# Performance work log

Hardware: AMD Instinct MI355X
Metric: run time of the kernel (lower is better)

## Reference

```python
import jax, jax.numpy as jnp
import numpy as np

N_QUBITS = 16
N_LAYERS = 4
N_ACTIONS = 6
BATCH = 512


def _apply_1q(state, U, wire):
    """Apply a single-qubit gate U to `wire` of batched state [B,2,...,2].
    U is [2,2] (shared) or [B,2,2] (per-sample)."""
    s = jnp.moveaxis(state, wire + 1, -1)
    if U.ndim == 2:
        s = jnp.einsum('ij,b...j->b...i', U, s)
    else:
        s = jnp.einsum('bij,b...j->b...i', U, s)
    return jnp.moveaxis(s, -1, wire + 1)


def _ry(theta):
    # RY(theta); theta scalar or [B]
    c = jnp.cos(theta / 2).astype(jnp.complex64)
    s = jnp.sin(theta / 2).astype(jnp.complex64)
    return jnp.stack([jnp.stack([c, -s], -1), jnp.stack([s, c], -1)], -2)


def _rot(phi, theta, omega):
    # PennyLane Rot = RZ(omega) RY(theta) RZ(phi)
    c = jnp.cos(theta / 2)
    s = jnp.sin(theta / 2)
    ep = jnp.exp(-0.5j * (phi + omega).astype(jnp.complex64))
    em = jnp.exp(-0.5j * (phi - omega).astype(jnp.complex64))
    m00 = ep * c
    m01 = -jnp.conj(em) * s
    m10 = em * s
    m11 = jnp.conj(ep) * c
    return jnp.stack([jnp.stack([m00, m01], -1), jnp.stack([m10, m11], -1)], -2)


def _cz_factor(wire):
    # diagonal CZ phase on wires (wire, wire+1): diag(1,1,1,-1)
    f = jnp.array([1, 1, 1, -1], dtype=jnp.complex64).reshape(2, 2)
    shape = (1,) + (1,) * wire + (2, 2) + (1,) * (N_QUBITS - wire - 2)
    return f.reshape(shape)


def _circuit(x, weights):
    # x: [B, n_qubits] angles; weights: [L, n_qubits, 3]
    B = x.shape[0]
    state = jnp.zeros((B,) + (2,) * N_QUBITS, dtype=jnp.complex64)
    state = state.at[(slice(None),) + (0,) * N_QUBITS].set(1.0)
    # AngleEmbedding: RY(x_i) on wire i (per-sample angles)
    for i in range(N_QUBITS):
        state = _apply_1q(state, _ry(x[:, i]), i)
    for l in range(N_LAYERS):
        for i in range(N_QUBITS):
            state = _apply_1q(state, _rot(weights[l, i, 0], weights[l, i, 1], weights[l, i, 2]), i)
        for i in range(N_QUBITS - 1):
            state = state * _cz_factor(i)
    probs = state.real ** 2 + state.imag ** 2  # [B,2,...,2]
    zs = []
    all_axes = tuple(range(1, N_QUBITS + 1))
    for i in range(N_QUBITS):
        pi = jnp.sum(probs, axis=tuple(a for a in all_axes if a != i + 1))  # [B,2]
        zs.append(pi[:, 0] - pi[:, 1])
    return jnp.stack(zs, axis=-1)  # [B, n_qubits] expval <Z_i>


def setup_inputs() -> dict:
    key = jax.random.key(0)
    k1, k2, k3, k4 = jax.random.split(key, 4)
    x = jax.random.uniform(k1, (BATCH, N_QUBITS), dtype=jnp.float32) * np.float32(np.pi)
    weights = jax.random.normal(k2, (N_LAYERS, N_QUBITS, 3), dtype=jnp.float32)
    fc_w = jax.random.normal(k3, (N_ACTIONS, N_QUBITS), dtype=jnp.float32) / np.float32(np.sqrt(N_QUBITS))
    fc_b = jax.random.normal(k4, (N_ACTIONS,), dtype=jnp.float32) * 0.01
    return {"x": x, "weights": weights, "fc_w": fc_w, "fc_b": fc_b}


def reference(x, weights, fc_w, fc_b):
    z = _circuit(x, weights).astype(jnp.float32)  # [B, n_qubits]
    return z @ fc_w.T + fc_b  # [B, n_actions]
```

## Files before the change

### kernel.cpp

```cpp
#include <hip/hip_runtime.h>

#define N_QUBITS 16
#define N_LAYERS 4
#define N_ACTIONS 6
#define BATCH 512


__global__ __launch_bounds__(1024, 4)
void qdqn_fused_kernel(const float* __restrict__ x,
                       const float* __restrict__ wt,
                       const float* __restrict__ fw,
                       const float* __restrict__ fb,
                       float* __restrict__ out)
{
    __shared__ float4 mats[4][N_QUBITS][2];
    __shared__ float zsh[N_QUBITS];

    const int tid = threadIdx.x;
    const int b   = blockIdx.x;

    if (tid < 64) {
        const int w = tid & 15;
        const int g = tid >> 4;
        float4 M0, M1;
        if (g == 0) {
            const float phi = wt[(0 * N_QUBITS + w) * 3 + 0];
            const float th  = wt[(0 * N_QUBITS + w) * 3 + 1];
            float sp, cp, st, ct;
            sincosf(0.5f * phi, &sp, &cp);
            sincosf(0.5f * th,  &st, &ct);
            const float w00r =  ct * cp, w00i = -ct * sp;
            const float w01r = -st * cp, w01i = -st * sp;
            const float w10r =  st * cp, w10i = -st * sp;
            const float w11r =  ct * cp, w11i =  ct * sp;
            float sx, cx;
            sincosf(0.5f * x[b * N_QUBITS + w], &sx, &cx);
            M0.x =  w00r * cx + w01r * sx;  M0.y =  w00i * cx + w01i * sx;
            M0.z = -w00r * sx + w01r * cx;  M0.w = -w00i * sx + w01i * cx;
            M1.x =  w10r * cx + w11r * sx;  M1.y =  w10i * cx + w11i * sx;
            M1.z = -w10r * sx + w11r * cx;  M1.w = -w10i * sx + w11i * cx;
        } else {
            const float al = wt[((g - 1) * N_QUBITS + w) * 3 + 2]
                           + wt[(g * N_QUBITS + w) * 3 + 0];
            const float th = wt[(g * N_QUBITS + w) * 3 + 1];
            float sa, ca, st, ct;
            sincosf(0.5f * al, &sa, &ca);
            sincosf(0.5f * th, &st, &ct);
            M0 = make_float4( ct * ca, -ct * sa, -st * ca, -st * sa);
            M1 = make_float4( st * ca, -st * sa,  ct * ca,  ct * sa);
        }
        mats[g][w][0] = M0;
        mats[g][w][1] = M1;
    }
    __syncthreads();

    const int lane = tid & 63;
    const int qi   = tid >> 6;
    int s = qi - 3;
    s = s < 0 ? 0 : (s > N_QUBITS - 7 ? N_QUBITS - 7 : s);
    const int jm = qi - s;

    float ar0 = (lane == 0) ? 1.0f : 0.0f, ai0 = 0.0f;
    float ar1 = 0.0f, ai1 = 0.0f;

    const int n0 = lane << 1, n1 = n0 | 1;
    const float czs0 = (__popc((n0 & (n0 >> 1)) & 0x3F) & 1) ? -1.0f : 1.0f;
    const float czs1 = (__popc((n1 & (n1 >> 1)) & 0x3F) & 1) ? -1.0f : 1.0f;

    auto applyM = [&](int j, float4 m0, float4 m1) {
        if (j == 0) {
            const float nr0 = m0.x*ar0 - m0.y*ai0 + m0.z*ar1 - m0.w*ai1;
            const float ni0 = m0.x*ai0 + m0.y*ar0 + m0.z*ai1 + m0.w*ar1;
            const float nr1 = m1.x*ar0 - m1.y*ai0 + m1.z*ar1 - m1.w*ai1;
            const float ni1 = m1.x*ai0 + m1.y*ar0 + m1.z*ai1 + m1.w*ar1;
            ar0 = nr0; ai0 = ni0; ar1 = nr1; ai1 = ni1;
        } else {
            const int  m  = 1 << (j - 1);
            const bool hi = (lane & m) != 0;
            const float dr = hi ? m1.z : m0.x;
            const float di = hi ? m1.w : m0.y;
            const float og = hi ? m1.x : m0.z;
            const float oi = hi ? m1.y : m0.w;
            {
                const float pr = __shfl_xor(ar0, m, 64);
                const float pi = __shfl_xor(ai0, m, 64);
                const float nr = dr*ar0 - di*ai0 + og*pr - oi*pi;
                const float ni = dr*ai0 + di*ar0 + og*pi + oi*pr;
                ar0 = nr; ai0 = ni;
            }
            {
                const float pr = __shfl_xor(ar1, m, 64);
                const float pi = __shfl_xor(ai1, m, 64);
                const float nr = dr*ar1 - di*ai1 + og*pr - oi*pi;
                const float ni = dr*ai1 + di*ar1 + og*pi + oi*pr;
                ar1 = nr; ai1 = ni;
            }
        }
    };

#pragma unroll
    for (int l = 0; l < 4; ++l) {
        const int rad = 3 - l;
#pragma unroll
        for (int dj = -3; dj <= 3; ++dj) {
            if (dj < -rad || dj > rad) continue;
            const int j = jm + dj;
            if (j >= 0 && j <= 6) {
                const int w = s + j;
                applyM(j, mats[l][w][0], mats[l][w][1]);
            }
        }
        if (l < 3) { ar0 *= czs0; ai0 *= czs0; ar1 *= czs1; ai1 *= czs1; }
    }

    const float sm0 = ((n0 >> jm) & 1) ? -1.0f : 1.0f;
    const float sm1 = ((n1 >> jm) & 1) ? -1.0f : 1.0f;
    float p = sm0 * (ar0*ar0 + ai0*ai0) + sm1 * (ar1*ar1 + ai1*ai1);
#pragma unroll
    for (int off = 32; off > 0; off >>= 1)
        p += __shfl_xor(p, off, 64);
    if (lane == 0) zsh[qi] = p;
    __syncthreads();

    if (tid < N_ACTIONS) {
        float acc = fb[tid];
#pragma unroll
        for (int i = 0; i < N_QUBITS; ++i)
            acc += zsh[i] * fw[tid * N_QUBITS + i];
        out[b * N_ACTIONS + tid] = acc;
    }
}

extern "C" void kernel_launch(void* const* d_in, const int* in_sizes, int n_in,
                              void* d_out, int out_size, void* d_ws, size_t ws_size,
                              hipStream_t stream) {
    const float* x    = (const float*)d_in[0];
    const float* wts  = (const float*)d_in[1];
    const float* fc_w = (const float*)d_in[2];
    const float* fc_b = (const float*)d_in[3];
    float* out = (float*)d_out;

    qdqn_fused_kernel<<<BATCH, 1024, 0, stream>>>(x, wts, fc_w, fc_b, out);
}
```

Baseline: 68.14 us.

## Split into prep kernel and 4-block-per-sample main kernel with atomic output

Gate matrix computation moves into a separate prep kernel that writes the per-sample first-layer matrices and the shared later-layer matrices to workspace, and also initialises the output with the bias. The main kernel now launches 2048 blocks of 256 threads, four blocks per sample, each handling four qubits' light-cone simulation. It loads matrices from workspace, applies the gates through fully unrolled macros with row-indexed matrix loads, and accumulates partial FC results with atomicAdd. This aims to improve occupancy and scheduling granularity, and to remove the redundant per-block trig work. In exchange it adds a second launch, workspace traffic, and atomics whose summation order is nondeterministic.

```diff
diff --git a/kernel.cpp b/kernel.cpp
--- a/kernel.cpp
+++ b/kernel.cpp
@@ -1,64 +1,78 @@
 #include <hip/hip_runtime.h>
 
-#define N_QUBITS 16
-#define N_LAYERS 4
-#define N_ACTIONS 6
+#define NQ 16
+#define NL 4
+#define NA 6
 #define BATCH 512
 
+#define A1_OFF 1024
 
-__global__ __launch_bounds__(1024, 4)
-void qdqn_fused_kernel(const float* __restrict__ x,
-                       const float* __restrict__ wt,
-                       const float* __restrict__ fw,
-                       const float* __restrict__ fb,
-                       float* __restrict__ out)
+__global__ __launch_bounds__(256)
+void prep_kernel(const float* __restrict__ x,
+                 const float* __restrict__ wt,
+                 const float* __restrict__ fb,
+                 float4* __restrict__ ws,
+                 float* __restrict__ out)
 {
-    __shared__ float4 mats[4][N_QUBITS][2];
-    __shared__ float zsh[N_QUBITS];
-
-    const int tid = threadIdx.x;
-    const int b   = blockIdx.x;
-
-    if (tid < 64) {
-        const int w = tid & 15;
-        const int g = tid >> 4;
-        float4 M0, M1;
-        if (g == 0) {
-            const float phi = wt[(0 * N_QUBITS + w) * 3 + 0];
-            const float th  = wt[(0 * N_QUBITS + w) * 3 + 1];
-            float sp, cp, st, ct;
-            sincosf(0.5f * phi, &sp, &cp);
-            sincosf(0.5f * th,  &st, &ct);
-            const float w00r =  ct * cp, w00i = -ct * sp;
-            const float w01r = -st * cp, w01i = -st * sp;
-            const float w10r =  st * cp, w10i = -st * sp;
-            const float w11r =  ct * cp, w11i =  ct * sp;
-            float sx, cx;
-            sincosf(0.5f * x[b * N_QUBITS + w], &sx, &cx);
-            M0.x =  w00r * cx + w01r * sx;  M0.y =  w00i * cx + w01i * sx;
-            M0.z = -w00r * sx + w01r * cx;  M0.w = -w00i * sx + w01i * cx;
-            M1.x =  w10r * cx + w11r * sx;  M1.y =  w10i * cx + w11i * sx;
-            M1.z = -w10r * sx + w11r * cx;  M1.w = -w10i * sx + w11i * cx;
-        } else {
-            const float al = wt[((g - 1) * N_QUBITS + w) * 3 + 2]
-                           + wt[(g * N_QUBITS + w) * 3 + 0];
-            const float th = wt[(g * N_QUBITS + w) * 3 + 1];
+    const int tid = threadIdx.x, blk = blockIdx.x;
+    if (blk < 32) {
+        const int t = blk * 256 + tid;
+        const int b = t >> 4, w = t & 15;
+        const float phi = wt[w * 3 + 0], th = wt[w * 3 + 1];
+        float sp, cp, st, ct, sx, cx;
+        sincosf(0.5f * phi, &sp, &cp);
+        sincosf(0.5f * th,  &st, &ct);
+        sincosf(0.5f * x[b * NQ + w], &sx, &cx);
+        const float w00r =  ct * cp, w00i = -ct * sp;
+        const float w01r = -st * cp, w01i = -st * sp;
+        const float w10r =  st * cp, w10i = -st * sp;
+        const float w11r =  ct * cp, w11i =  ct * sp;
+        const float a00r =  w00r * cx + w01r * sx, a00i =  w00i * cx + w01i * sx;
+        const float a01r = -w00r * sx + w01r * cx, a01i = -w00i * sx + w01i * cx;
+        const float a10r =  w10r * cx + w11r * sx, a10i =  w10i * cx + w11i * sx;
+        const float a11r = -w10r * sx + w11r * cx, a11i = -w10i * sx + w11i * cx;
+        ws[A1_OFF + t * 2 + 0] = make_float4(a00r, a00i, a01r, a01i);
+        ws[A1_OFF + t * 2 + 1] = make_float4(a11r, a11i, a10r, a10i);
+    } else if (blk == 32) {
+        if (tid < 48) {
+            const int g = tid >> 4, w = tid & 15;
+            const int l = g + 1;
+            const float al = wt[((l - 1) * NQ + w) * 3 + 2] + wt[(l * NQ + w) * 3 + 0];
+            const float th = wt[(l * NQ + w) * 3 + 1];
             float sa, ca, st, ct;
             sincosf(0.5f * al, &sa, &ca);
             sincosf(0.5f * th, &st, &ct);
-            M0 = make_float4( ct * ca, -ct * sa, -st * ca, -st * sa);
-            M1 = make_float4( st * ca, -st * sa,  ct * ca,  ct * sa);
+            ws[tid * 2 + 0] = make_float4(ct * ca, -ct * sa, -st * ca, -st * sa);
+            ws[tid * 2 + 1] = make_float4(ct * ca,  ct * sa,  st * ca, -st * sa);
         }
-        mats[g][w][0] = M0;
-        mats[g][w][1] = M1;
+    } else {
+        const int t = (blk - 33) * 256 + tid;
+        if (t < BATCH * NA) out[t] = fb[t - (t / NA) * NA];
+    }
+}
+
+
+__global__ __launch_bounds__(256, 8)
+void qmain_kernel(const float4* __restrict__ ws,
+                  const float* __restrict__ fw,
+                  float* __restrict__ out)
+{
+    __shared__ float4 lm[4][NQ][2];
+    __shared__ float zsh[4];
+
+    const int tid = threadIdx.x;
+    const int b   = blockIdx.x >> 2;
+
+    if (tid < 128) {
+        const int g = tid >> 5;
+        ((float4*)lm)[tid] = (g == 0) ? ws[A1_OFF + (b << 5) + tid]
+                                      : ws[tid - 32];
     }
     __syncthreads();
 
     const int lane = tid & 63;
-    const int qi   = tid >> 6;
-    int s = qi - 3;
-    s = s < 0 ? 0 : (s > N_QUBITS - 7 ? N_QUBITS - 7 : s);
-    const int jm = qi - s;
+    const int wv   = tid >> 6;
+    const int qi   = ((blockIdx.x & 3) << 2) | wv;
 
     float ar0 = (lane == 0) ? 1.0f : 0.0f, ai0 = 0.0f;
     float ar1 = 0.0f, ai1 = 0.0f;
@@ -67,67 +81,60 @@
     const float czs0 = (__popc((n0 & (n0 >> 1)) & 0x3F) & 1) ? -1.0f : 1.0f;
     const float czs1 = (__popc((n1 & (n1 >> 1)) & 0x3F) & 1) ? -1.0f : 1.0f;
 
-    auto applyM = [&](int j, float4 m0, float4 m1) {
-        if (j == 0) {
-            const float nr0 = m0.x*ar0 - m0.y*ai0 + m0.z*ar1 - m0.w*ai1;
-            const float ni0 = m0.x*ai0 + m0.y*ar0 + m0.z*ai1 + m0.w*ar1;
-            const float nr1 = m1.x*ar0 - m1.y*ai0 + m1.z*ar1 - m1.w*ai1;
-            const float ni1 = m1.x*ai0 + m1.y*ar0 + m1.z*ai1 + m1.w*ar1;
-            ar0 = nr0; ai0 = ni0; ar1 = nr1; ai1 = ni1;
-        } else {
-            const int  m  = 1 << (j - 1);
-            const bool hi = (lane & m) != 0;
-            const float dr = hi ? m1.z : m0.x;
-            const float di = hi ? m1.w : m0.y;
-            const float og = hi ? m1.x : m0.z;
-            const float oi = hi ? m1.y : m0.w;
-            {
-                const float pr = __shfl_xor(ar0, m, 64);
-                const float pi = __shfl_xor(ai0, m, 64);
-                const float nr = dr*ar0 - di*ai0 + og*pr - oi*pi;
-                const float ni = dr*ai0 + di*ar0 + og*pi + oi*pr;
-                ar0 = nr; ai0 = ni;
-            }
-            {
-                const float pr = __shfl_xor(ar1, m, 64);
-                const float pi = __shfl_xor(ai1, m, 64);
-                const float nr = dr*ar1 - di*ai1 + og*pr - oi*pi;
-                const float ni = dr*ai1 + di*ar1 + og*pi + oi*pr;
-                ar1 = nr; ai1 = ni;
-            }
-        }
-    };
+#define GATE(J, G) do {                                                        \
+    const int w_ = qi + (J) - 3;                                               \
+    if (0 <= w_ && w_ < NQ) {                                                  \
+        if ((J) == 0) {                                                        \
+            const float4 r0 = lm[G][w_][0], r1 = lm[G][w_][1];                 \
+            const float nr0 = r0.x*ar0 - r0.y*ai0 + r0.z*ar1 - r0.w*ai1;       \
+            const float ni0 = r0.x*ai0 + r0.y*ar0 + r0.z*ai1 + r0.w*ar1;       \
+            const float nr1 = r1.z*ar0 - r1.w*ai0 + r1.x*ar1 - r1.y*ai1;       \
+            const float ni1 = r1.z*ai0 + r1.w*ar0 + r1.x*ai1 + r1.y*ar1;       \
+            ar0 = nr0; ai0 = ni0; ar1 = nr1; ai1 = ni1;                        \
+        } else {                                                               \
+            const int m_   = 1 << ((J) - 1);                                   \
+            const int row_ = (lane >> ((J) - 1)) & 1;                          \
+            const float4 c = lm[G][w_][row_];                                  \
+            const float pr0 = __shfl_xor(ar0, m_, 64);                         \
+            const float pi0 = __shfl_xor(ai0, m_, 64);                         \
+            const float pr1 = __shfl_xor(ar1, m_, 64);                         \
+            const float pi1 = __shfl_xor(ai1, m_, 64);                         \
+            const float t0r = c.x*ar0 - c.y*ai0 + c.z*pr0 - c.w*pi0;           \
+            const float t0i = c.x*ai0 + c.y*ar0 + c.z*pi0 + c.w*pr0;           \
+            const float t1r = c.x*ar1 - c.y*ai1 + c.z*pr1 - c.w*pi1;           \
+            const float t1i = c.x*ai1 + c.y*ar1 + c.z*pi1 + c.w*pr1;           \
+            ar0 = t0r; ai0 = t0i; ar1 = t1r; ai1 = t1i;                        \
+        }                                                                      \
+    }                                                                          \
+} while (0)
 
-#pragma unroll
-    for (int l = 0; l < 4; ++l) {
-        const int rad = 3 - l;
-#pragma unroll
-        for (int dj = -3; dj <= 3; ++dj) {
-            if (dj < -rad || dj > rad) continue;
-            const int j = jm + dj;
-            if (j >= 0 && j <= 6) {
-                const int w = s + j;
-                applyM(j, mats[l][w][0], mats[l][w][1]);
-            }
-        }
-        if (l < 3) { ar0 *= czs0; ai0 *= czs0; ar1 *= czs1; ai1 *= czs1; }
-    }
+#define CZ() do { ar0 *= czs0; ai0 *= czs0; ar1 *= czs1; ai1 *= czs1; } while (0)
 
-    const float sm0 = ((n0 >> jm) & 1) ? -1.0f : 1.0f;
-    const float sm1 = ((n1 >> jm) & 1) ? -1.0f : 1.0f;
-    float p = sm0 * (ar0*ar0 + ai0*ai0) + sm1 * (ar1*ar1 + ai1*ai1);
+    GATE(0,0); GATE(1,0); GATE(2,0); GATE(3,0); GATE(4,0); GATE(5,0); GATE(6,0);
+    CZ();
+    GATE(1,1); GATE(2,1); GATE(3,1); GATE(4,1); GATE(5,1);
+    CZ();
+    GATE(2,2); GATE(3,2); GATE(4,2);
+    CZ();
+    GATE(3,3);
+
+#undef GATE
+#undef CZ
+
+    const float sm = ((lane >> 2) & 1) ? -1.0f : 1.0f;
+    float p = sm * (ar0*ar0 + ai0*ai0 + ar1*ar1 + ai1*ai1);
 #pragma unroll
     for (int off = 32; off > 0; off >>= 1)
         p += __shfl_xor(p, off, 64);
-    if (lane == 0) zsh[qi] = p;
+
+    if (lane == 0) zsh[wv] = p;
     __syncthreads();
 
-    if (tid < N_ACTIONS) {
-        float acc = fb[tid];
-#pragma unroll
-        for (int i = 0; i < N_QUBITS; ++i)
-            acc += zsh[i] * fw[tid * N_QUBITS + i];
-        out[b * N_ACTIONS + tid] = acc;
+    if (tid < NA) {
+        const int q0 = (blockIdx.x & 3) << 2;
+        const float* fwr = fw + tid * NQ + q0;
+        const float acc = zsh[0]*fwr[0] + zsh[1]*fwr[1] + zsh[2]*fwr[2] + zsh[3]*fwr[3];
+        atomicAdd(&out[b * NA + tid], acc);
     }
 }
 
@@ -138,7 +145,9 @@
     const float* wts  = (const float*)d_in[1];
     const float* fc_w = (const float*)d_in[2];
     const float* fc_b = (const float*)d_in[3];
-    float* out = (float*)d_out;
+    float* out  = (float*)d_out;
+    float4* ws4 = (float4*)d_ws;
 
-    qdqn_fused_kernel<<<BATCH, 1024, 0, stream>>>(x, wts, fc_w, fc_b, out);
+    prep_kernel<<<45, 256, 0, stream>>>(x, wts, fc_b, ws4, out);
+    qmain_kernel<<<2048, 256, 0, stream>>>(ws4, fc_w, out);
 }
```

Result: no change. 68.84 us (+1.0%).
